# Performance work log

Measured on AMD Instinct MI355X. Metric: run time of the kernel, lower is better.

Reference implementation:

```python
import jax, jax.numpy as jnp
import numpy as np

B = 512      # batch
T = 128      # decoder horizon -> T-1 = 127 steps
DNH = 128    # decoder_num_hidden
ENC = 2 * DNH   # encoder_num_hidden (required by attn concat: 3*ENC == 6*DNH)
H = 2 * DNH     # LSTM hidden size


def setup_inputs() -> dict:
    key = jax.random.key(0)
    ks = jax.random.split(key, 10)
    def w(k, shape, scale=0.05):
        return jax.random.normal(k, shape, jnp.float32) * scale
    return {
        "X_encoded": jax.random.normal(ks[0], (B, T - 1, ENC), jnp.float32),
        "y_prev":    jax.random.normal(ks[1], (B, T - 1), jnp.float32),
        # attn_layer: Linear(6*DNH -> DNH) then Linear(DNH -> 1)
        "W_attn1": w(ks[2], (DNH, 6 * DNH)), "b_attn1": jnp.zeros((DNH,), jnp.float32),
        "W_attn2": w(ks[3], (1, DNH)),       "b_attn2": jnp.zeros((1,), jnp.float32),
        # fc: Linear(2*DNH+1 -> 1)
        "W_fc": w(ks[4], (1, 2 * DNH + 1)),  "b_fc": jnp.zeros((1,), jnp.float32),
        # single-layer LSTM, input_size=1, hidden=H, PyTorch gate order (i,f,g,o)
        "W_ih": w(ks[5], (4 * H, 1)), "W_hh": w(ks[6], (4 * H, H)),
        "b_ih": jnp.zeros((4 * H,), jnp.float32), "b_hh": jnp.zeros((4 * H,), jnp.float32),
        # fc_final: Linear(4*DNH -> 1)
        "W_final": w(ks[7], (1, 4 * DNH)), "b_final": jnp.zeros((1,), jnp.float32),
    }


def reference(X_encoded, y_prev, W_attn1, b_attn1, W_attn2, b_attn2,
              W_fc, b_fc, W_ih, W_hh, b_ih, b_hh, W_final, b_final):
    Bz, Tm1, E = X_encoded.shape
    Hh = W_hh.shape[1]
    d0 = jnp.zeros((Bz, Hh), X_encoded.dtype)
    c0 = jnp.zeros((Bz, Hh), X_encoded.dtype)

    def step(carry, y_t):
        d, c = carry                                   # (B, H) each
        state = jnp.concatenate([d, c], axis=-1)[:, None, :]        # (B,1,2H)
        x = jnp.concatenate(
            [jnp.broadcast_to(state, (Bz, Tm1, 2 * Hh)), X_encoded], axis=-1)  # (B,T-1,6*DNH)
        a = x @ W_attn1.T + b_attn1                    # (B,T-1,DNH)
        score = (a @ W_attn2.T + b_attn2)[..., 0]      # (B,T-1)
        beta = jax.nn.softmax(score, axis=1)
        context = jnp.einsum('bt,bte->be', beta, X_encoded)          # (B,E)
        y = jnp.concatenate([context, y_t[:, None]], axis=-1)        # (B,E+1)
        y_tilde = y @ W_fc.T + b_fc                    # (B,1)
        gates = y_tilde @ W_ih.T + b_ih + d @ W_hh.T + b_hh          # (B,4H)
        i, f, g, o = jnp.split(gates, 4, axis=-1)
        i, f, o = jax.nn.sigmoid(i), jax.nn.sigmoid(f), jax.nn.sigmoid(o)
        g = jnp.tanh(g)
        c_new = f * c + i * g
        d_new = o * jnp.tanh(c_new)
        return (d_new, c_new), context

    (dT, _), contexts = jax.lax.scan(step, (d0, c0), y_prev.T)
    y_pred = jnp.concatenate([dT, contexts[-1]], axis=-1) @ W_final.T + b_final  # (B,1)
    return y_pred
```

## Files before the change

### kernel.cpp

```cpp
#include <hip/hip_runtime.h>
#include <stdint.h>

typedef __attribute__((ext_vector_type(8))) short short8;
typedef __attribute__((ext_vector_type(8))) unsigned short ushort8_t;
typedef __attribute__((ext_vector_type(4))) float floatx4;

#define T1 127
#define ENC 256
#define HD 256

#define WHI_OFF   0u
#define WLO_OFF   524288u
#define D0_OFF    1048576u
#define D1_OFF    1572864u
#define WEFF_OFF  2097152u
#define YT_OFF    2099200u
#define CTX_OFF   2361344u
#define DT_OFF    2885632u

__device__ __forceinline__ void split_bf16(float x, unsigned& hi, unsigned& lo) {
    unsigned u = __float_as_uint(x);
    hi = u >> 16;
    float hf = __uint_as_float(hi << 16);
    float r = x - hf;
    unsigned ur = __float_as_uint(r);
    lo = (ur + 0x7fffu + ((ur >> 16) & 1u)) >> 16;
}

__device__ __forceinline__ float sigm_f(float x) { return 1.f / (1.f + __expf(-x)); }
__device__ __forceinline__ float tanh_f(float x) {
    x = fminf(9.f, fmaxf(-9.f, x));
    float e = __expf(2.f * x);
    return (e - 1.f) / (e + 1.f);
}

__device__ __forceinline__ void load64_ag(const unsigned long long* p,
                                          uint4& a, uint4& b, uint4& c, uint4& d) {
    asm volatile("global_load_dwordx4 %0, %4, off sc0 sc1\n\t"
                 "global_load_dwordx4 %1, %4, off offset:16 sc0 sc1\n\t"
                 "global_load_dwordx4 %2, %4, off offset:32 sc0 sc1\n\t"
                 "global_load_dwordx4 %3, %4, off offset:48 sc0 sc1\n\t"
                 "s_waitcnt vmcnt(0)"
                 : "=v"(a), "=v"(b), "=v"(c), "=v"(d)
                 : "v"((unsigned long long)p)
                 : "memory");
}

__global__ __launch_bounds__(256) void k_prep(const float* __restrict__ W1,
                                              const float* __restrict__ W2,
                                              const float* __restrict__ W_hh,
                                              char* __restrict__ ws) {
    const int tid = threadIdx.x, bid = blockIdx.x;
    ushort* Whi = (ushort*)(ws + WHI_OFF);
    ushort* Wlo = (ushort*)(ws + WLO_OFF);
    {
        const int i4 = bid * 256 + tid;
        float4 v = ((const float4*)W_hh)[i4];
        float vv[4] = {v.x, v.y, v.z, v.w};
        unsigned h[4], l[4];
        #pragma unroll
        for (int j = 0; j < 4; ++j) split_bf16(vv[j], h[j], l[j]);
        *(ushort4*)(Whi + i4 * 4) = make_ushort4((ushort)h[0], (ushort)h[1], (ushort)h[2], (ushort)h[3]);
        *(ushort4*)(Wlo + i4 * 4) = make_ushort4((ushort)l[0], (ushort)l[1], (ushort)l[2], (ushort)l[3]);
    }
    {
        const int idx = bid * 256 + tid;
        if (idx < 32768) ((uint4*)(ws + D0_OFF))[idx] = make_uint4(0, 0, 0, 0);
    }
    if (bid == 0) {
        float acc = 0.f;
        for (int j = 0; j < 128; ++j)
            acc = fmaf(W2[j], W1[j * 768 + 512 + tid], acc);
        ((float*)(ws + WEFF_OFF))[tid] = acc;
    }
}

__global__ __launch_bounds__(512) void k_attn(const float* __restrict__ X,
                                              const float* __restrict__ y_prev,
                                              const float* __restrict__ W_fc,
                                              const float* __restrict__ b_fc,
                                              char* __restrict__ ws) {
    __shared__ float s_lds[128];
    __shared__ float beta[128];
    __shared__ float part[512];
    __shared__ float wsum[8];
    __shared__ float su;
    const int b = blockIdx.x, tid = threadIdx.x;
    const int w = tid >> 6, lane = tid & 63;
    const float* Xb = X + (size_t)b * T1 * ENC;
    const float* weff = (const float*)(ws + WEFF_OFF);
    const float4 w4 = ((const float4*)weff)[lane];
    #pragma unroll 4
    for (int i = 0; i < 16; ++i) {
        int t = w * 16 + i;
        if (t >= T1) break;
        float4 x4 = ((const float4*)(Xb + t * ENC))[lane];
        float a = x4.x * w4.x + x4.y * w4.y + x4.z * w4.z + x4.w * w4.w;
        for (int m = 32; m >= 1; m >>= 1) a += __shfl_xor(a, m, 64);
        if (lane == 0) s_lds[t] = a;
    }
    __syncthreads();
    if (w == 0) {
        float v0 = s_lds[lane];
        float v1 = (lane + 64 < T1) ? s_lds[lane + 64] : -1e30f;
        float mx = fmaxf(v0, v1);
        for (int m = 32; m >= 1; m >>= 1) mx = fmaxf(mx, __shfl_xor(mx, m, 64));
        float e0 = __expf(v0 - mx);
        float e1 = (lane + 64 < T1) ? __expf(v1 - mx) : 0.f;
        float s = e0 + e1;
        for (int m = 32; m >= 1; m >>= 1) s += __shfl_xor(s, m, 64);
        float inv = 1.f / s;
        beta[lane] = e0 * inv;
        if (lane + 64 < T1) beta[lane + 64] = e1 * inv;
    }
    __syncthreads();
    {
        const int col = tid & 255, half = tid >> 8;
        const int t0 = half * 64;
        const int tend = half ? T1 : 64;
        float acc = 0.f;
        for (int t = t0; t < tend; ++t) acc = fmaf(beta[t], Xb[t * ENC + col], acc);
        part[half * 256 + col] = acc;
    }
    __syncthreads();
    float v = 0.f;
    if (tid < 256) {
        float ctx = part[tid] + part[256 + tid];
        ((float*)(ws + CTX_OFF))[b * ENC + tid] = ctx;
        v = ctx * W_fc[tid];
    }
    for (int m = 32; m >= 1; m >>= 1) v += __shfl_xor(v, m, 64);
    if (lane == 0) wsum[w] = v;
    __syncthreads();
    if (tid == 0)
        su = wsum[0] + wsum[1] + wsum[2] + wsum[3] + b_fc[0];
    __syncthreads();
    const float wy = W_fc[256];
    if (tid < T1)
        ((float*)(ws + YT_OFF))[b * 128 + tid] = su + wy * y_prev[b * T1 + tid];
}

__global__ __launch_bounds__(256, 1) void k_lstm(const float* __restrict__ W_ih,
                                                 const float* __restrict__ b_ih,
                                                 const float* __restrict__ b_hh,
                                                 char* __restrict__ ws) {
    __shared__ __align__(16) ushort ldh[16 * 264];
    __shared__ __align__(16) ushort ldl[16 * 264];
    __shared__ float gbuf[16 * 132];

    const int tid = threadIdx.x, bid = blockIdx.x;
    const int gi = bid >> 3, hj = bid & 7;
    const int w = tid >> 6, lane = tid & 63;
    const int n16 = lane & 15, q = lane >> 4;

    const ushort* Whi = (const ushort*)(ws + WHI_OFF);
    const ushort* Wlo = (const ushort*)(ws + WLO_OFF);
    unsigned long long* Dbuf0 = (unsigned long long*)(ws + D0_OFF);
    unsigned long long* Dbuf1 = (unsigned long long*)(ws + D1_OFF);
    const float* yt = (const float*)(ws + YT_OFF);
    float* dT = (float*)(ws + DT_OFF);

    short8 bfh[2][8], bfl[2][8];
    #pragma unroll
    for (int j = 0; j < 2; ++j) {
        const int r = (2 * w + j) * 16 + n16;
        const int hloc = r >> 2, g = r & 3;
        const int R = g * 256 + hj * 32 + hloc;
        #pragma unroll
        for (int kt = 0; kt < 8; ++kt) {
            bfh[j][kt] = *(const short8*)(Whi + R * 256 + kt * 32 + q * 8);
            bfl[j][kt] = *(const short8*)(Wlo + R * 256 + kt * 32 + q * 8);
        }
    }

    const int b_loc = tid & 15, hpair = tid >> 4;
    const int hloc0 = hpair * 2;
    const int bg = gi * 16 + b_loc;
    float wihr[2][4], bihr[2][4];
    #pragma unroll
    for (int jj = 0; jj < 2; ++jj)
        #pragma unroll
        for (int g = 0; g < 4; ++g) {
            const int row = g * HD + hj * 32 + hloc0 + jj;
            wihr[jj][g] = W_ih[row];
            bihr[jj][g] = b_ih[row] + b_hh[row];
        }
    float cc0 = 0.f, cc1 = 0.f;

    const int pb = tid >> 4, hp8 = tid & 15;
    const bool own = ((hp8 >> 1) == hj);
    const size_t pbase = (size_t)(gi * 16 + pb) * 128 + hp8 * 8;

    {
        ushort8_t z = {0, 0, 0, 0, 0, 0, 0, 0};
        *(ushort8_t*)(ldh + pb * 264 + hp8 * 16)     = z;
        *(ushort8_t*)(ldh + pb * 264 + hp8 * 16 + 8) = z;
        *(ushort8_t*)(ldl + pb * 264 + hp8 * 16)     = z;
        *(ushort8_t*)(ldl + pb * 264 + hp8 * 16 + 8) = z;
    }

    for (int t = 1; t <= T1; ++t) {
        const float ytv = yt[bg * 128 + (t - 1)];
        if (!own) {
            unsigned long long* Dsrc = ((t - 1) & 1) ? Dbuf1 : Dbuf0;
            const unsigned e = (unsigned)(t - 1) & 3u;
            unsigned lo[8], hi[8];
            for (int round = 0; ; ++round) {
                uint4 A, B, C, D;
                load64_ag(&Dsrc[pbase], A, B, C, D);
                lo[0] = A.x; hi[0] = A.y; lo[1] = A.z; hi[1] = A.w;
                lo[2] = B.x; hi[2] = B.y; lo[3] = B.z; hi[3] = B.w;
                lo[4] = C.x; hi[4] = C.y; lo[5] = C.z; hi[5] = C.w;
                lo[6] = D.x; hi[6] = D.y; lo[7] = D.z; hi[7] = D.w;
                bool ok = true;
                #pragma unroll
                for (int i = 0; i < 8; ++i) {
                    unsigned ep = (lo[i] & 1u) | ((hi[i] & 1u) << 1);
                    ok &= (ep == e);
                }
                if (ok) break;
                if (round >= 16) __builtin_amdgcn_s_sleep(1);
            }
            ushort hv[16], lv[16];
            #pragma unroll
            for (int i = 0; i < 8; ++i) {
                hv[2 * i]     = (ushort)(lo[i] >> 16);
                hv[2 * i + 1] = (ushort)(hi[i] >> 16);
                lv[2 * i]     = (ushort)(lo[i] & 0xFFFEu);
                lv[2 * i + 1] = (ushort)(hi[i] & 0xFFFEu);
            }
            ushort8_t H0, L0, H1, L1;
            #pragma unroll
            for (int i = 0; i < 8; ++i) { H0[i] = hv[i]; L0[i] = lv[i]; H1[i] = hv[8 + i]; L1[i] = lv[8 + i]; }
            *(ushort8_t*)(ldh + pb * 264 + hp8 * 16)     = H0;
            *(ushort8_t*)(ldh + pb * 264 + hp8 * 16 + 8) = H1;
            *(ushort8_t*)(ldl + pb * 264 + hp8 * 16)     = L0;
            *(ushort8_t*)(ldl + pb * 264 + hp8 * 16 + 8) = L1;
        }
        __syncthreads();
        floatx4 acc0 = {0.f, 0.f, 0.f, 0.f}, acc1 = {0.f, 0.f, 0.f, 0.f};
        #pragma unroll
        for (int kt = 0; kt < 8; ++kt) {
            short8 ah = *(const short8*)(ldh + n16 * 264 + kt * 32 + q * 8);
            short8 al = *(const short8*)(ldl + n16 * 264 + kt * 32 + q * 8);
            acc0 = __builtin_amdgcn_mfma_f32_16x16x32_bf16(ah, bfh[0][kt], acc0, 0, 0, 0);
            acc0 = __builtin_amdgcn_mfma_f32_16x16x32_bf16(al, bfh[0][kt], acc0, 0, 0, 0);
            acc0 = __builtin_amdgcn_mfma_f32_16x16x32_bf16(ah, bfl[0][kt], acc0, 0, 0, 0);
            acc1 = __builtin_amdgcn_mfma_f32_16x16x32_bf16(ah, bfh[1][kt], acc1, 0, 0, 0);
            acc1 = __builtin_amdgcn_mfma_f32_16x16x32_bf16(al, bfh[1][kt], acc1, 0, 0, 0);
            acc1 = __builtin_amdgcn_mfma_f32_16x16x32_bf16(ah, bfl[1][kt], acc1, 0, 0, 0);
        }
        #pragma unroll
        for (int reg = 0; reg < 4; ++reg) {
            gbuf[(q * 4 + reg) * 132 + (2 * w) * 16 + n16]     = acc0[reg];
            gbuf[(q * 4 + reg) * 132 + (2 * w + 1) * 16 + n16] = acc1[reg];
        }
        __syncthreads();
        float dnew[2];
        #pragma unroll
        for (int jj = 0; jj < 2; ++jj) {
            const int base = b_loc * 132 + (hloc0 + jj) * 4;
            float pi = gbuf[base + 0] + ytv * wihr[jj][0] + bihr[jj][0];
            float pf = gbuf[base + 1] + ytv * wihr[jj][1] + bihr[jj][1];
            float pg = gbuf[base + 2] + ytv * wihr[jj][2] + bihr[jj][2];
            float po = gbuf[base + 3] + ytv * wihr[jj][3] + bihr[jj][3];
            float ig = sigm_f(pi), fg = sigm_f(pf), og = sigm_f(po);
            float gg = tanh_f(pg);
            float& c = jj ? cc1 : cc0;
            c = fg * c + ig * gg;
            dnew[jj] = og * tanh_f(c);
        }
        if (t < T1) {
            const unsigned e = (unsigned)t & 3u;
            unsigned h0, l0, h1, l1;
            split_bf16(dnew[0], h0, l0);
            split_bf16(dnew[1], h1, l1);
            l0 = (l0 & 0xFFFEu) | (e & 1u);
            l1 = (l1 & 0xFFFEu) | ((e >> 1) & 1u);
            unsigned long long wv = ((unsigned long long)h1 << 48) |
                                    ((unsigned long long)l1 << 32) |
                                    ((unsigned long long)h0 << 16) |
                                    (unsigned long long)l0;
            unsigned long long* Ddst = (t & 1) ? Dbuf1 : Dbuf0;
            __hip_atomic_store(&Ddst[(size_t)bg * 128 + hj * 16 + hpair], wv,
                               __ATOMIC_RELAXED, __HIP_MEMORY_SCOPE_AGENT);
            *(ushort2*)(ldh + b_loc * 264 + hj * 32 + hloc0) =
                make_ushort2((ushort)h0, (ushort)h1);
            *(ushort2*)(ldl + b_loc * 264 + hj * 32 + hloc0) =
                make_ushort2((ushort)(l0 & 0xFFFEu), (ushort)(l1 & 0xFFFEu));
        } else {
            *(float2*)(dT + bg * 256 + hj * 32 + hloc0) = make_float2(dnew[0], dnew[1]);
        }
    }
}

__global__ __launch_bounds__(256) void k_final(const float* __restrict__ W_final,
                                               const float* __restrict__ b_final,
                                               float* __restrict__ out,
                                               char* __restrict__ ws) {
    __shared__ float red[256];
    const int b = blockIdx.x, tid = threadIdx.x;
    const float* dT = (const float*)(ws + DT_OFF);
    const float* ctx = (const float*)(ws + CTX_OFF);
    float v = W_final[tid] * dT[b * 256 + tid] + W_final[256 + tid] * ctx[b * 256 + tid];
    red[tid] = v;
    __syncthreads();
    for (int s = 128; s >= 1; s >>= 1) { if (tid < s) red[tid] += red[tid + s]; __syncthreads(); }
    if (tid == 0) out[b] = red[0] + b_final[0];
}

extern "C" void kernel_launch(void* const* d_in, const int* in_sizes, int n_in,
                              void* d_out, int out_size, void* d_ws, size_t ws_size,
                              hipStream_t stream) {
    const float* X      = (const float*)d_in[0];
    const float* y_prev = (const float*)d_in[1];
    const float* W1     = (const float*)d_in[2];
    const float* W2     = (const float*)d_in[4];
    const float* W_fc   = (const float*)d_in[6];
    const float* b_fc   = (const float*)d_in[7];
    const float* W_ih   = (const float*)d_in[8];
    const float* W_hh   = (const float*)d_in[9];
    const float* b_ih   = (const float*)d_in[10];
    const float* b_hh   = (const float*)d_in[11];
    const float* W_fin  = (const float*)d_in[12];
    const float* b_fin  = (const float*)d_in[13];
    char* ws = (char*)d_ws;

    hipLaunchKernelGGL(k_prep,  dim3(256), dim3(256), 0, stream, W1, W2, W_hh, ws);
    hipLaunchKernelGGL(k_attn,  dim3(512), dim3(512), 0, stream, X, y_prev, W_fc, b_fc, ws);
    hipLaunchKernelGGL(k_lstm,  dim3(256), dim3(256), 0, stream, W_ih, b_ih, b_hh, ws);
    hipLaunchKernelGGL(k_final, dim3(512), dim3(256), 0, stream, W_fin, b_fin, (float*)d_out, ws);
}
```

Baseline: 547.7 us.

## Load hidden state directly into MFMA operands per wave, drop LDS staging and barriers

Each wave in the LSTM kernel now polls the published hidden state straight from global memory into registers laid out as MFMA A-operands. This removes the LDS staging of the state and both block-wide __syncthreads per step. Gate results now go through a per-wave LDS buffer, and a lane shuffle pairs outputs for publishing. The W_hh hi/lo bf16 split also moves from the prep kernel into the LSTM kernel's register preload. The cost is that every wave issues 16 global loads per poll instead of a shared, partitioned load, which adds L2 traffic and per-wave spin latency.

```diff
diff --git a/kernel.cpp b/kernel.cpp
--- a/kernel.cpp
+++ b/kernel.cpp
@@ -2,15 +2,12 @@
 #include <stdint.h>
 
 typedef __attribute__((ext_vector_type(8))) short short8;
-typedef __attribute__((ext_vector_type(8))) unsigned short ushort8_t;
 typedef __attribute__((ext_vector_type(4))) float floatx4;
 
 #define T1 127
 #define ENC 256
 #define HD 256
 
-#define WHI_OFF   0u
-#define WLO_OFF   524288u
 #define D0_OFF    1048576u
 #define D1_OFF    1572864u
 #define WEFF_OFF  2097152u
@@ -34,35 +31,10 @@
     return (e - 1.f) / (e + 1.f);
 }
 
-__device__ __forceinline__ void load64_ag(const unsigned long long* p,
-                                          uint4& a, uint4& b, uint4& c, uint4& d) {
-    asm volatile("global_load_dwordx4 %0, %4, off sc0 sc1\n\t"
-                 "global_load_dwordx4 %1, %4, off offset:16 sc0 sc1\n\t"
-                 "global_load_dwordx4 %2, %4, off offset:32 sc0 sc1\n\t"
-                 "global_load_dwordx4 %3, %4, off offset:48 sc0 sc1\n\t"
-                 "s_waitcnt vmcnt(0)"
-                 : "=v"(a), "=v"(b), "=v"(c), "=v"(d)
-                 : "v"((unsigned long long)p)
-                 : "memory");
-}
-
 __global__ __launch_bounds__(256) void k_prep(const float* __restrict__ W1,
                                               const float* __restrict__ W2,
-                                              const float* __restrict__ W_hh,
                                               char* __restrict__ ws) {
     const int tid = threadIdx.x, bid = blockIdx.x;
-    ushort* Whi = (ushort*)(ws + WHI_OFF);
-    ushort* Wlo = (ushort*)(ws + WLO_OFF);
-    {
-        const int i4 = bid * 256 + tid;
-        float4 v = ((const float4*)W_hh)[i4];
-        float vv[4] = {v.x, v.y, v.z, v.w};
-        unsigned h[4], l[4];
-        #pragma unroll
-        for (int j = 0; j < 4; ++j) split_bf16(vv[j], h[j], l[j]);
-        *(ushort4*)(Whi + i4 * 4) = make_ushort4((ushort)h[0], (ushort)h[1], (ushort)h[2], (ushort)h[3]);
-        *(ushort4*)(Wlo + i4 * 4) = make_ushort4((ushort)l[0], (ushort)l[1], (ushort)l[2], (ushort)l[3]);
-    }
     {
         const int idx = bid * 256 + tid;
         if (idx < 32768) ((uint4*)(ws + D0_OFF))[idx] = make_uint4(0, 0, 0, 0);
@@ -143,18 +115,15 @@
 __global__ __launch_bounds__(256, 1) void k_lstm(const float* __restrict__ W_ih,
                                                  const float* __restrict__ b_ih,
                                                  const float* __restrict__ b_hh,
+                                                 const float* __restrict__ W_hh,
                                                  char* __restrict__ ws) {
-    __shared__ __align__(16) ushort ldh[16 * 264];
-    __shared__ __align__(16) ushort ldl[16 * 264];
-    __shared__ float gbuf[16 * 132];
+    __shared__ float gbufw[4][16 * 36];
 
     const int tid = threadIdx.x, bid = blockIdx.x;
     const int gi = bid >> 3, hj = bid & 7;
     const int w = tid >> 6, lane = tid & 63;
     const int n16 = lane & 15, q = lane >> 4;
 
-    const ushort* Whi = (const ushort*)(ws + WHI_OFF);
-    const ushort* Wlo = (const ushort*)(ws + WLO_OFF);
     unsigned long long* Dbuf0 = (unsigned long long*)(ws + D0_OFF);
     unsigned long long* Dbuf1 = (unsigned long long*)(ws + D1_OFF);
     const float* yt = (const float*)(ws + YT_OFF);
@@ -168,128 +137,150 @@
         const int R = g * 256 + hj * 32 + hloc;
         #pragma unroll
         for (int kt = 0; kt < 8; ++kt) {
-            bfh[j][kt] = *(const short8*)(Whi + R * 256 + kt * 32 + q * 8);
-            bfl[j][kt] = *(const short8*)(Wlo + R * 256 + kt * 32 + q * 8);
-        }
-    }
-
-    const int b_loc = tid & 15, hpair = tid >> 4;
-    const int hloc0 = hpair * 2;
+            const float* src = W_hh + R * 256 + kt * 32 + q * 8;
+            float4 f0 = ((const float4*)src)[0];
+            float4 f1 = ((const float4*)src)[1];
+            float vv[8] = {f0.x, f0.y, f0.z, f0.w, f1.x, f1.y, f1.z, f1.w};
+            unsigned h[8], l[8];
+            #pragma unroll
+            for (int i = 0; i < 8; ++i) split_bf16(vv[i], h[i], l[i]);
+            short8 sh, sl;
+            #pragma unroll
+            for (int i = 0; i < 8; ++i) { sh[i] = (short)h[i]; sl[i] = (short)l[i]; }
+            bfh[j][kt] = sh;
+            bfl[j][kt] = sl;
+        }
+    }
+
+    const int jb = n16 & 3, sa = n16 >> 2;
+    const int b_loc = q * 4 + jb;
     const int bg = gi * 16 + b_loc;
+    const int hlA = 8 * w + sa, hlB = hlA + 4;
     float wihr[2][4], bihr[2][4];
     #pragma unroll
-    for (int jj = 0; jj < 2; ++jj)
-        #pragma unroll
-        for (int g = 0; g < 4; ++g) {
-            const int row = g * HD + hj * 32 + hloc0 + jj;
-            wihr[jj][g] = W_ih[row];
-            bihr[jj][g] = b_ih[row] + b_hh[row];
-        }
+    for (int g = 0; g < 4; ++g) {
+        const int rowA = g * HD + hj * 32 + hlA;
+        const int rowB = g * HD + hj * 32 + hlB;
+        wihr[0][g] = W_ih[rowA]; bihr[0][g] = b_ih[rowA] + b_hh[rowA];
+        wihr[1][g] = W_ih[rowB]; bihr[1][g] = b_ih[rowB] + b_hh[rowB];
+    }
     float cc0 = 0.f, cc1 = 0.f;
 
-    const int pb = tid >> 4, hp8 = tid & 15;
-    const bool own = ((hp8 >> 1) == hj);
-    const size_t pbase = (size_t)(gi * 16 + pb) * 128 + hp8 * 8;
-
-    {
-        ushort8_t z = {0, 0, 0, 0, 0, 0, 0, 0};
-        *(ushort8_t*)(ldh + pb * 264 + hp8 * 16)     = z;
-        *(ushort8_t*)(ldh + pb * 264 + hp8 * 16 + 8) = z;
-        *(ushort8_t*)(ldl + pb * 264 + hp8 * 16)     = z;
-        *(ushort8_t*)(ldl + pb * 264 + hp8 * 16 + 8) = z;
-    }
+    const size_t base_w = (size_t)(gi * 16 + n16) * 128 + q * 4;
+
+    const int hpair = (sa & 1) ? (4 * w + 2 + (sa >> 1)) : (4 * w + (sa >> 1));
+    const size_t pub_idx = (size_t)bg * 128 + hj * 16 + hpair;
+
+    float* gb = gbufw[w];
 
     for (int t = 1; t <= T1; ++t) {
         const float ytv = yt[bg * 128 + (t - 1)];
-        if (!own) {
-            unsigned long long* Dsrc = ((t - 1) & 1) ? Dbuf1 : Dbuf0;
-            const unsigned e = (unsigned)(t - 1) & 3u;
-            unsigned lo[8], hi[8];
-            for (int round = 0; ; ++round) {
-                uint4 A, B, C, D;
-                load64_ag(&Dsrc[pbase], A, B, C, D);
-                lo[0] = A.x; hi[0] = A.y; lo[1] = A.z; hi[1] = A.w;
-                lo[2] = B.x; hi[2] = B.y; lo[3] = B.z; hi[3] = B.w;
-                lo[4] = C.x; hi[4] = C.y; lo[5] = C.z; hi[5] = C.w;
-                lo[6] = D.x; hi[6] = D.y; lo[7] = D.z; hi[7] = D.w;
-                bool ok = true;
-                #pragma unroll
-                for (int i = 0; i < 8; ++i) {
-                    unsigned ep = (lo[i] & 1u) | ((hi[i] & 1u) << 1);
-                    ok &= (ep == e);
-                }
-                if (ok) break;
-                if (round >= 16) __builtin_amdgcn_s_sleep(1);
-            }
-            ushort hv[16], lv[16];
-            #pragma unroll
-            for (int i = 0; i < 8; ++i) {
-                hv[2 * i]     = (ushort)(lo[i] >> 16);
-                hv[2 * i + 1] = (ushort)(hi[i] >> 16);
-                lv[2 * i]     = (ushort)(lo[i] & 0xFFFEu);
-                lv[2 * i + 1] = (ushort)(hi[i] & 0xFFFEu);
-            }
-            ushort8_t H0, L0, H1, L1;
-            #pragma unroll
-            for (int i = 0; i < 8; ++i) { H0[i] = hv[i]; L0[i] = lv[i]; H1[i] = hv[8 + i]; L1[i] = lv[8 + i]; }
-            *(ushort8_t*)(ldh + pb * 264 + hp8 * 16)     = H0;
-            *(ushort8_t*)(ldh + pb * 264 + hp8 * 16 + 8) = H1;
-            *(ushort8_t*)(ldl + pb * 264 + hp8 * 16)     = L0;
-            *(ushort8_t*)(ldl + pb * 264 + hp8 * 16 + 8) = L1;
-        }
-        __syncthreads();
+        unsigned long long* Dsrc = ((t - 1) & 1) ? Dbuf1 : Dbuf0;
+        const unsigned e  = (unsigned)(t - 1) & 3u;
+        const unsigned eh = e >> 1;
+        const unsigned long long addr = (unsigned long long)(Dsrc + base_w);
+        uint4 a0, b0, a1, b1, a2, b2, a3, b3, a4, b4, a5, b5, a6, b6, a7, b7;
+        for (int round = 0; ; ++round) {
+            asm volatile(
+                "global_load_dwordx4 %0, %16, off sc0 sc1\n\t"
+                "global_load_dwordx4 %1, %16, off offset:16 sc0 sc1\n\t"
+                "global_load_dwordx4 %2, %16, off offset:128 sc0 sc1\n\t"
+                "global_load_dwordx4 %3, %16, off offset:144 sc0 sc1\n\t"
+                "global_load_dwordx4 %4, %16, off offset:256 sc0 sc1\n\t"
+                "global_load_dwordx4 %5, %16, off offset:272 sc0 sc1\n\t"
+                "global_load_dwordx4 %6, %16, off offset:384 sc0 sc1\n\t"
+                "global_load_dwordx4 %7, %16, off offset:400 sc0 sc1\n\t"
+                "global_load_dwordx4 %8, %16, off offset:512 sc0 sc1\n\t"
+                "global_load_dwordx4 %9, %16, off offset:528 sc0 sc1\n\t"
+                "global_load_dwordx4 %10, %16, off offset:640 sc0 sc1\n\t"
+                "global_load_dwordx4 %11, %16, off offset:656 sc0 sc1\n\t"
+                "global_load_dwordx4 %12, %16, off offset:768 sc0 sc1\n\t"
+                "global_load_dwordx4 %13, %16, off offset:784 sc0 sc1\n\t"
+                "global_load_dwordx4 %14, %16, off offset:896 sc0 sc1\n\t"
+                "global_load_dwordx4 %15, %16, off offset:912 sc0 sc1\n\t"
+                "s_waitcnt vmcnt(0)"
+                : "=&v"(a0), "=&v"(b0), "=&v"(a1), "=&v"(b1),
+                  "=&v"(a2), "=&v"(b2), "=&v"(a3), "=&v"(b3),
+                  "=&v"(a4), "=&v"(b4), "=&v"(a5), "=&v"(b5),
+                  "=&v"(a6), "=&v"(b6), "=&v"(a7), "=&v"(b7)
+                : "v"(addr) : "memory");
+            unsigned bad = 0;
+#define CHK(A, B) bad |= (A.x ^ e) | (A.z ^ e) | (B.x ^ e) | (B.z ^ e) | \
+                         (A.y ^ eh) | (A.w ^ eh) | (B.y ^ eh) | (B.w ^ eh)
+            CHK(a0, b0); CHK(a1, b1); CHK(a2, b2); CHK(a3, b3);
+            CHK(a4, b4); CHK(a5, b5); CHK(a6, b6); CHK(a7, b7);
+#undef CHK
+            if (__all((bad & 1u) == 0u)) break;
+            if (round >= 8) __builtin_amdgcn_s_sleep(1);
+        }
         floatx4 acc0 = {0.f, 0.f, 0.f, 0.f}, acc1 = {0.f, 0.f, 0.f, 0.f};
-        #pragma unroll
-        for (int kt = 0; kt < 8; ++kt) {
-            short8 ah = *(const short8*)(ldh + n16 * 264 + kt * 32 + q * 8);
-            short8 al = *(const short8*)(ldl + n16 * 264 + kt * 32 + q * 8);
-            acc0 = __builtin_amdgcn_mfma_f32_16x16x32_bf16(ah, bfh[0][kt], acc0, 0, 0, 0);
-            acc0 = __builtin_amdgcn_mfma_f32_16x16x32_bf16(al, bfh[0][kt], acc0, 0, 0, 0);
-            acc0 = __builtin_amdgcn_mfma_f32_16x16x32_bf16(ah, bfl[0][kt], acc0, 0, 0, 0);
-            acc1 = __builtin_amdgcn_mfma_f32_16x16x32_bf16(ah, bfh[1][kt], acc1, 0, 0, 0);
-            acc1 = __builtin_amdgcn_mfma_f32_16x16x32_bf16(al, bfh[1][kt], acc1, 0, 0, 0);
-            acc1 = __builtin_amdgcn_mfma_f32_16x16x32_bf16(ah, bfl[1][kt], acc1, 0, 0, 0);
-        }
+#define KT(A, B, kt) { \
+            union { int4 i; short8 s; } uh_, ul_; \
+            uh_.i.x = (int)((A.y & 0xffff0000u) | (A.x >> 16)); \
+            uh_.i.y = (int)((A.w & 0xffff0000u) | (A.z >> 16)); \
+            uh_.i.z = (int)((B.y & 0xffff0000u) | (B.x >> 16)); \
+            uh_.i.w = (int)((B.w & 0xffff0000u) | (B.z >> 16)); \
+            ul_.i.x = (int)(((A.y & 0xfffeu) << 16) | (A.x & 0xfffeu)); \
+            ul_.i.y = (int)(((A.w & 0xfffeu) << 16) | (A.z & 0xfffeu)); \
+            ul_.i.z = (int)(((B.y & 0xfffeu) << 16) | (B.x & 0xfffeu)); \
+            ul_.i.w = (int)(((B.w & 0xfffeu) << 16) | (B.z & 0xfffeu)); \
+            acc0 = __builtin_amdgcn_mfma_f32_16x16x32_bf16(uh_.s, bfh[0][kt], acc0, 0, 0, 0); \
+            acc0 = __builtin_amdgcn_mfma_f32_16x16x32_bf16(ul_.s, bfh[0][kt], acc0, 0, 0, 0); \
+            acc0 = __builtin_amdgcn_mfma_f32_16x16x32_bf16(uh_.s, bfl[0][kt], acc0, 0, 0, 0); \
+            acc1 = __builtin_amdgcn_mfma_f32_16x16x32_bf16(uh_.s, bfh[1][kt], acc1, 0, 0, 0); \
+            acc1 = __builtin_amdgcn_mfma_f32_16x16x32_bf16(ul_.s, bfh[1][kt], acc1, 0, 0, 0); \
+            acc1 = __builtin_amdgcn_mfma_f32_16x16x32_bf16(uh_.s, bfl[1][kt], acc1, 0, 0, 0); }
+        KT(a0, b0, 0); KT(a1, b1, 1); KT(a2, b2, 2); KT(a3, b3, 3);
+        KT(a4, b4, 4); KT(a5, b5, 5); KT(a6, b6, 6); KT(a7, b7, 7);
+#undef KT
         #pragma unroll
         for (int reg = 0; reg < 4; ++reg) {
-            gbuf[(q * 4 + reg) * 132 + (2 * w) * 16 + n16]     = acc0[reg];
-            gbuf[(q * 4 + reg) * 132 + (2 * w + 1) * 16 + n16] = acc1[reg];
-        }
-        __syncthreads();
-        float dnew[2];
-        #pragma unroll
-        for (int jj = 0; jj < 2; ++jj) {
-            const int base = b_loc * 132 + (hloc0 + jj) * 4;
-            float pi = gbuf[base + 0] + ytv * wihr[jj][0] + bihr[jj][0];
-            float pf = gbuf[base + 1] + ytv * wihr[jj][1] + bihr[jj][1];
-            float pg = gbuf[base + 2] + ytv * wihr[jj][2] + bihr[jj][2];
-            float po = gbuf[base + 3] + ytv * wihr[jj][3] + bihr[jj][3];
+            gb[(q * 4 + reg) * 36 + n16]      = acc0[reg];
+            gb[(q * 4 + reg) * 36 + 16 + n16] = acc1[reg];
+        }
+        asm volatile("s_waitcnt lgkmcnt(0)" ::: "memory");
+        float4 gA = *(const float4*)&gb[b_loc * 36 + sa * 4];
+        float4 gB = *(const float4*)&gb[b_loc * 36 + 16 + sa * 4];
+        float dn0, dn1;
+        {
+            float pi = gA.x + ytv * wihr[0][0] + bihr[0][0];
+            float pf = gA.y + ytv * wihr[0][1] + bihr[0][1];
+            float pg = gA.z + ytv * wihr[0][2] + bihr[0][2];
+            float po = gA.w + ytv * wihr[0][3] + bihr[0][3];
             float ig = sigm_f(pi), fg = sigm_f(pf), og = sigm_f(po);
-            float gg = tanh_f(pg);
-            float& c = jj ? cc1 : cc0;
-            c = fg * c + ig * gg;
-            dnew[jj] = og * tanh_f(c);
-        }
+            cc0 = fg * cc0 + ig * tanh_f(pg);
+            dn0 = og * tanh_f(cc0);
+        }
+        {
+            float pi = gB.x + ytv * wihr[1][0] + bihr[1][0];
+            float pf = gB.y + ytv * wihr[1][1] + bihr[1][1];
+            float pg = gB.z + ytv * wihr[1][2] + bihr[1][2];
+            float po = gB.w + ytv * wihr[1][3] + bihr[1][3];
+            float ig = sigm_f(pi), fg = sigm_f(pf), og = sigm_f(po);
+            cc1 = fg * cc1 + ig * tanh_f(pg);
+            dn1 = og * tanh_f(cc1);
+        }
+        float r0 = __shfl_xor(dn0, 4, 64);
+        float r1 = __shfl_xor(dn1, 4, 64);
+        float de, do_;
+        if (sa & 1) { de = r1; do_ = dn1; } else { de = dn0; do_ = r0; }
         if (t < T1) {
-            const unsigned e = (unsigned)t & 3u;
-            unsigned h0, l0, h1, l1;
-            split_bf16(dnew[0], h0, l0);
-            split_bf16(dnew[1], h1, l1);
-            l0 = (l0 & 0xFFFEu) | (e & 1u);
-            l1 = (l1 & 0xFFFEu) | ((e >> 1) & 1u);
-            unsigned long long wv = ((unsigned long long)h1 << 48) |
-                                    ((unsigned long long)l1 << 32) |
-                                    ((unsigned long long)h0 << 16) |
-                                    (unsigned long long)l0;
+            const unsigned ep = (unsigned)t & 3u;
+            unsigned he, le, ho, lo_;
+            split_bf16(de, he, le);
+            split_bf16(do_, ho, lo_);
+            le  = (le  & 0xFFFEu) | (ep & 1u);
+            lo_ = (lo_ & 0xFFFEu) | ((ep >> 1) & 1u);
+            unsigned long long wv = ((unsigned long long)ho << 48) |
+                                    ((unsigned long long)lo_ << 32) |
+                                    ((unsigned long long)he << 16) |
+                                    (unsigned long long)le;
             unsigned long long* Ddst = (t & 1) ? Dbuf1 : Dbuf0;
-            __hip_atomic_store(&Ddst[(size_t)bg * 128 + hj * 16 + hpair], wv,
-                               __ATOMIC_RELAXED, __HIP_MEMORY_SCOPE_AGENT);
-            *(ushort2*)(ldh + b_loc * 264 + hj * 32 + hloc0) =
-                make_ushort2((ushort)h0, (ushort)h1);
-            *(ushort2*)(ldl + b_loc * 264 + hj * 32 + hloc0) =
-                make_ushort2((ushort)(l0 & 0xFFFEu), (ushort)(l1 & 0xFFFEu));
+            __hip_atomic_store(&Ddst[pub_idx], wv, __ATOMIC_RELAXED,
+                               __HIP_MEMORY_SCOPE_AGENT);
         } else {
-            *(float2*)(dT + bg * 256 + hj * 32 + hloc0) = make_float2(dnew[0], dnew[1]);
+            *(float2*)(dT + (size_t)bg * 256 + hj * 32 + 2 * hpair) =
+                make_float2(de, do_);
         }
     }
 }
@@ -326,8 +317,8 @@
     const float* b_fin  = (const float*)d_in[13];
     char* ws = (char*)d_ws;
 
-    hipLaunchKernelGGL(k_prep,  dim3(256), dim3(256), 0, stream, W1, W2, W_hh, ws);
+    hipLaunchKernelGGL(k_prep,  dim3(128), dim3(256), 0, stream, W1, W2, ws);
     hipLaunchKernelGGL(k_attn,  dim3(512), dim3(512), 0, stream, X, y_prev, W_fc, b_fc, ws);
-    hipLaunchKernelGGL(k_lstm,  dim3(256), dim3(256), 0, stream, W_ih, b_ih, b_hh, ws);
+    hipLaunchKernelGGL(k_lstm,  dim3(256), dim3(256), 0, stream, W_ih, b_ih, b_hh, W_hh, ws);
     hipLaunchKernelGGL(k_final, dim3(512), dim3(256), 0, stream, W_fin, b_fin, (float*)d_out, ws);
 }
```

Result: slower. 1.038 ms (+89.5%).

## Fold prep and final kernels into attention and LSTM kernels

Applied to the files above, without the earlier changes.

Removes the separate prep and final-reduction kernels. The weff projection is now computed per block inside the attention kernel, and the W_hh hi/lo bf16 split is done directly in LSTM register loading. Each LSTM block also zeroes its own D0 slot. The output is assembled by the attention kernel writing the context term, plus atomicAdds of the final hidden-state dot product from LSTM blocks. This saves two launches and workspace round-trips, at the cost of redundant weff computation in every attention block and float atomic ordering nondeterminism. The self-zeroing of D0 may race with other blocks' reads if there is no synchronisation before the first step.

```diff
diff --git a/kernel.cpp b/kernel.cpp
--- a/kernel.cpp
+++ b/kernel.cpp
@@ -9,14 +9,9 @@
 #define ENC 256
 #define HD 256
 
-#define WHI_OFF   0u
-#define WLO_OFF   524288u
 #define D0_OFF    1048576u
 #define D1_OFF    1572864u
-#define WEFF_OFF  2097152u
 #define YT_OFF    2099200u
-#define CTX_OFF   2361344u
-#define DT_OFF    2885632u
 
 __device__ __forceinline__ void split_bf16(float x, unsigned& hi, unsigned& lo) {
     unsigned u = __float_as_uint(x);
@@ -46,50 +41,38 @@
                  : "memory");
 }
 
-__global__ __launch_bounds__(256) void k_prep(const float* __restrict__ W1,
-                                              const float* __restrict__ W2,
-                                              const float* __restrict__ W_hh,
-                                              char* __restrict__ ws) {
-    const int tid = threadIdx.x, bid = blockIdx.x;
-    ushort* Whi = (ushort*)(ws + WHI_OFF);
-    ushort* Wlo = (ushort*)(ws + WLO_OFF);
-    {
-        const int i4 = bid * 256 + tid;
-        float4 v = ((const float4*)W_hh)[i4];
-        float vv[4] = {v.x, v.y, v.z, v.w};
-        unsigned h[4], l[4];
-        #pragma unroll
-        for (int j = 0; j < 4; ++j) split_bf16(vv[j], h[j], l[j]);
-        *(ushort4*)(Whi + i4 * 4) = make_ushort4((ushort)h[0], (ushort)h[1], (ushort)h[2], (ushort)h[3]);
-        *(ushort4*)(Wlo + i4 * 4) = make_ushort4((ushort)l[0], (ushort)l[1], (ushort)l[2], (ushort)l[3]);
-    }
-    {
-        const int idx = bid * 256 + tid;
-        if (idx < 32768) ((uint4*)(ws + D0_OFF))[idx] = make_uint4(0, 0, 0, 0);
-    }
-    if (bid == 0) {
-        float acc = 0.f;
-        for (int j = 0; j < 128; ++j)
-            acc = fmaf(W2[j], W1[j * 768 + 512 + tid], acc);
-        ((float*)(ws + WEFF_OFF))[tid] = acc;
-    }
-}
-
 __global__ __launch_bounds__(512) void k_attn(const float* __restrict__ X,
                                               const float* __restrict__ y_prev,
+                                              const float* __restrict__ W1,
+                                              const float* __restrict__ W2,
                                               const float* __restrict__ W_fc,
                                               const float* __restrict__ b_fc,
+                                              const float* __restrict__ W_final,
+                                              const float* __restrict__ b_final,
+                                              float* __restrict__ out,
                                               char* __restrict__ ws) {
     __shared__ float s_lds[128];
     __shared__ float beta[128];
     __shared__ float part[512];
     __shared__ float wsum[8];
+    __shared__ float fsum[8];
     __shared__ float su;
     const int b = blockIdx.x, tid = threadIdx.x;
     const int w = tid >> 6, lane = tid & 63;
     const float* Xb = X + (size_t)b * T1 * ENC;
-    const float* weff = (const float*)(ws + WEFF_OFF);
-    const float4 w4 = ((const float4*)weff)[lane];
+    float4 w4; w4.x = w4.y = w4.z = w4.w = 0.f;
+    {
+        const float* W1c = W1 + 512 + lane * 4;
+        #pragma unroll 4
+        for (int j = 0; j < 128; ++j) {
+            const float s = W2[j];
+            const float4 c = *(const float4*)(W1c + j * 768);
+            w4.x = fmaf(s, c.x, w4.x);
+            w4.y = fmaf(s, c.y, w4.y);
+            w4.z = fmaf(s, c.z, w4.z);
+            w4.w = fmaf(s, c.w, w4.w);
+        }
+    }
     #pragma unroll 4
     for (int i = 0; i < 16; ++i) {
         int t = w * 16 + i;
@@ -123,17 +106,22 @@
         part[half * 256 + col] = acc;
     }
     __syncthreads();
-    float v = 0.f;
+    float v = 0.f, vf = 0.f;
     if (tid < 256) {
         float ctx = part[tid] + part[256 + tid];
-        ((float*)(ws + CTX_OFF))[b * ENC + tid] = ctx;
-        v = ctx * W_fc[tid];
-    }
-    for (int m = 32; m >= 1; m >>= 1) v += __shfl_xor(v, m, 64);
-    if (lane == 0) wsum[w] = v;
-    __syncthreads();
-    if (tid == 0)
+        v  = ctx * W_fc[tid];
+        vf = ctx * W_final[256 + tid];
+    }
+    for (int m = 32; m >= 1; m >>= 1) {
+        v  += __shfl_xor(v, m, 64);
+        vf += __shfl_xor(vf, m, 64);
+    }
+    if (lane == 0) { wsum[w] = v; fsum[w] = vf; }
+    __syncthreads();
+    if (tid == 0) {
         su = wsum[0] + wsum[1] + wsum[2] + wsum[3] + b_fc[0];
+        out[b] = fsum[0] + fsum[1] + fsum[2] + fsum[3] + b_final[0];
+    }
     __syncthreads();
     const float wy = W_fc[256];
     if (tid < T1)
@@ -143,6 +131,9 @@
 __global__ __launch_bounds__(256, 1) void k_lstm(const float* __restrict__ W_ih,
                                                  const float* __restrict__ b_ih,
                                                  const float* __restrict__ b_hh,
+                                                 const float* __restrict__ W_hh,
+                                                 const float* __restrict__ W_final,
+                                                 float* __restrict__ out,
                                                  char* __restrict__ ws) {
     __shared__ __align__(16) ushort ldh[16 * 264];
     __shared__ __align__(16) ushort ldl[16 * 264];
@@ -153,12 +144,16 @@
     const int w = tid >> 6, lane = tid & 63;
     const int n16 = lane & 15, q = lane >> 4;
 
-    const ushort* Whi = (const ushort*)(ws + WHI_OFF);
-    const ushort* Wlo = (const ushort*)(ws + WLO_OFF);
     unsigned long long* Dbuf0 = (unsigned long long*)(ws + D0_OFF);
     unsigned long long* Dbuf1 = (unsigned long long*)(ws + D1_OFF);
     const float* yt = (const float*)(ws + YT_OFF);
-    float* dT = (float*)(ws + DT_OFF);
+
+    const int b_loc = tid & 15, hpair = tid >> 4;
+    const int hloc0 = hpair * 2;
+    const int bg = gi * 16 + b_loc;
+
+    __hip_atomic_store(&Dbuf0[(size_t)bg * 128 + hj * 16 + hpair], 0ull,
+                       __ATOMIC_RELAXED, __HIP_MEMORY_SCOPE_AGENT);
 
     short8 bfh[2][8], bfl[2][8];
     #pragma unroll
@@ -168,14 +163,21 @@
         const int R = g * 256 + hj * 32 + hloc;
         #pragma unroll
         for (int kt = 0; kt < 8; ++kt) {
-            bfh[j][kt] = *(const short8*)(Whi + R * 256 + kt * 32 + q * 8);
-            bfl[j][kt] = *(const short8*)(Wlo + R * 256 + kt * 32 + q * 8);
-        }
-    }
-
-    const int b_loc = tid & 15, hpair = tid >> 4;
-    const int hloc0 = hpair * 2;
-    const int bg = gi * 16 + b_loc;
+            const float* src = W_hh + R * 256 + kt * 32 + q * 8;
+            float4 f0 = ((const float4*)src)[0];
+            float4 f1 = ((const float4*)src)[1];
+            float vv[8] = {f0.x, f0.y, f0.z, f0.w, f1.x, f1.y, f1.z, f1.w};
+            unsigned h[8], l[8];
+            #pragma unroll
+            for (int i = 0; i < 8; ++i) split_bf16(vv[i], h[i], l[i]);
+            short8 sh, sl;
+            #pragma unroll
+            for (int i = 0; i < 8; ++i) { sh[i] = (short)h[i]; sl[i] = (short)l[i]; }
+            bfh[j][kt] = sh;
+            bfl[j][kt] = sl;
+        }
+    }
+
     float wihr[2][4], bihr[2][4];
     #pragma unroll
     for (int jj = 0; jj < 2; ++jj)
@@ -289,24 +291,11 @@
             *(ushort2*)(ldl + b_loc * 264 + hj * 32 + hloc0) =
                 make_ushort2((ushort)(l0 & 0xFFFEu), (ushort)(l1 & 0xFFFEu));
         } else {
-            *(float2*)(dT + bg * 256 + hj * 32 + hloc0) = make_float2(dnew[0], dnew[1]);
-        }
-    }
-}
-
-__global__ __launch_bounds__(256) void k_final(const float* __restrict__ W_final,
-                                               const float* __restrict__ b_final,
-                                               float* __restrict__ out,
-                                               char* __restrict__ ws) {
-    __shared__ float red[256];
-    const int b = blockIdx.x, tid = threadIdx.x;
-    const float* dT = (const float*)(ws + DT_OFF);
-    const float* ctx = (const float*)(ws + CTX_OFF);
-    float v = W_final[tid] * dT[b * 256 + tid] + W_final[256 + tid] * ctx[b * 256 + tid];
-    red[tid] = v;
-    __syncthreads();
-    for (int s = 128; s >= 1; s >>= 1) { if (tid < s) red[tid] += red[tid + s]; __syncthreads(); }
-    if (tid == 0) out[b] = red[0] + b_final[0];
+            const float wf0 = W_final[hj * 32 + hloc0];
+            const float wf1 = W_final[hj * 32 + hloc0 + 1];
+            atomicAdd(out + bg, dnew[0] * wf0 + dnew[1] * wf1);
+        }
+    }
 }
 
 extern "C" void kernel_launch(void* const* d_in, const int* in_sizes, int n_in,
@@ -326,8 +315,8 @@
     const float* b_fin  = (const float*)d_in[13];
     char* ws = (char*)d_ws;
 
-    hipLaunchKernelGGL(k_prep,  dim3(256), dim3(256), 0, stream, W1, W2, W_hh, ws);
-    hipLaunchKernelGGL(k_attn,  dim3(512), dim3(512), 0, stream, X, y_prev, W_fc, b_fc, ws);
-    hipLaunchKernelGGL(k_lstm,  dim3(256), dim3(256), 0, stream, W_ih, b_ih, b_hh, ws);
-    hipLaunchKernelGGL(k_final, dim3(512), dim3(256), 0, stream, W_fin, b_fin, (float*)d_out, ws);
-}
+    hipLaunchKernelGGL(k_attn, dim3(512), dim3(512), 0, stream,
+                       X, y_prev, W1, W2, W_fc, b_fc, W_fin, b_fin, (float*)d_out, ws);
+    hipLaunchKernelGGL(k_lstm, dim3(256), dim3(256), 0, stream,
+                       W_ih, b_ih, b_hh, W_hh, W_fin, (float*)d_out, ws);
+}
```

Measured after the change: 565.7 us. 1.03x slower.
